# Kernel optimization log

Measured on AMD Instinct MI355X. Metric: run time of the kernel, lower is better.

The kernel has to match this reference:

```python
import jax, jax.numpy as jnp
import numpy as np

DIM, HEADS, B, S = 128, 4, 8, 80
BN_SCALE = np.float32(1.0 / np.sqrt(1.0 + 1e-5))  # eval-mode BatchNorm2d with running stats (0, 1)


def conv2d(x, w, b=None, groups=1, pad=0):
    y = jax.lax.conv_general_dilated(x, w, (1, 1), [(pad, pad), (pad, pad)],
                                     dimension_numbers=('NCHW', 'OIHW', 'NCHW'),
                                     feature_group_count=groups)
    return y if b is None else y + b[None, :, None, None]


def gate(x, w1, b1, g, bt, w2, b2):
    # Conv1x1 -> BatchNorm2d(eval) -> ReLU -> Conv1x1 -> Sigmoid
    y = conv2d(x, w1, b1)
    y = y * (g * BN_SCALE)[None, :, None, None] + bt[None, :, None, None]
    return jax.nn.sigmoid(conv2d(jax.nn.relu(y), w2, b2))


def layernorm(x, w, b):
    # Restormer WithBias LayerNorm over the channel dim
    mu = jnp.mean(x, 1, keepdims=True)
    var = jnp.var(x, 1, keepdims=True)
    return (x - mu) / jnp.sqrt(var + 1e-5) * w[None, :, None, None] + b[None, :, None, None]


def l2norm(x):
    # F.normalize(dim=-1) incl. complex: divide by L2 norm of |x|
    n = jnp.sqrt(jnp.sum(jnp.abs(x) ** 2, -1, keepdims=True))
    return x / jnp.maximum(n, 1e-12)


def split_heads(t):
    b, c, h, w = t.shape
    return t.reshape(b, HEADS, c // HEADS, h * w)


def _etb(x, ln1_w, ln1_b, ln2_w, ln2_b,
         f_temp, f_proj_w, f_w1, f_wb1, f_bn_g, f_bn_b, f_w2, f_wb2,
         s_temp, s_q1_w, s_q1_b, s_k1_w, s_k1_b, s_v1_w, s_v1_b,
         s_q3_w, s_q5_w, s_k3_w, s_k5_w, s_v3_w, s_v5_w, s_c3_w, s_c5_w, s_proj_w,
         ff_dw1_w, ff_dw2_w, ff_proj_w,
         ffg_w1, ffg_b1, ffg_bng, ffg_bnb, ffg_w2, ffg_b2,
         ffg1_w1, ffg1_b1, ffg1_bng, ffg1_bnb, ffg1_w2, ffg1_b2):
    b, c, h, w = x.shape
    G = c // 2
    xn = layernorm(x, ln1_w, ln1_b)
    # ---- Attention_F (the repeated fft2(x) calls in torch are identical; computed once) ----
    xf = jnp.fft.fft2(xn)
    qf = l2norm(split_heads(xf))  # q_f == k_f in the original code
    vf = split_heads(xf)
    attn = jnp.einsum('bhcn,bhdn->bhcd', qf, qf) * f_temp
    attn = jax.nn.softmax(attn.real, -1) + 1j * jax.nn.softmax(attn.imag, -1)
    # NOTE: torch applies ifft2 over the LAST TWO dims of [b, head, c, h*w] -> (c, h*w)
    out_f = jnp.abs(jnp.fft.ifft2(jnp.einsum('bhcd,bhdn->bhcn', attn, vf))).reshape(b, c, h, w)
    out_f_l = jnp.abs(jnp.fft.ifft2(gate(xf.real, f_w1, f_wb1, f_bn_g, f_bn_b, f_w2, f_wb2) * xf))
    a_f = conv2d(jnp.concatenate([out_f, out_f_l], 1), f_proj_w)
    # ---- Attention_S ----
    q1 = conv2d(xn, s_q1_w, s_q1_b)
    k1 = conv2d(xn, s_k1_w, s_k1_b)
    v1 = conv2d(xn, s_v1_w, s_v1_b)
    qs = jnp.concatenate([conv2d(q1, s_q3_w, groups=G, pad=1), conv2d(q1, s_q5_w, groups=G, pad=2)], 1)
    ks = jnp.concatenate([conv2d(k1, s_k3_w, groups=G, pad=1), conv2d(k1, s_k5_w, groups=G, pad=2)], 1)
    vs = jnp.concatenate([conv2d(v1, s_v3_w, groups=G, pad=1), conv2d(v1, s_v5_w, groups=G, pad=2)], 1)
    qn = l2norm(split_heads(qs))
    kn = l2norm(split_heads(ks))
    vh = split_heads(vs)
    attn_s = jax.nn.softmax(jnp.einsum('bhcn,bhdn->bhcd', qn, kn) * s_temp, -1)
    out_s = jnp.einsum('bhcd,bhdn->bhcn', attn_s, vh).reshape(b, c, h, w)
    out_s_l = jnp.concatenate([conv2d(xn, s_c3_w, groups=G, pad=1), conv2d(xn, s_c5_w, groups=G, pad=2)], 1)
    a_s = conv2d(jnp.concatenate([out_s, out_s_l], 1), s_proj_w)
    x = x + a_f + a_s
    # ---- FeedForward ----
    xn2 = layernorm(x, ln2_w, ln2_b)
    xf2 = jnp.fft.fft2(xn2)
    x_f = jnp.abs(gate(xf2.real, ffg_w1, ffg_b1, ffg_bng, ffg_bnb, ffg_w2, ffg_b2) * xf2)
    x_f_g = jax.nn.gelu(x_f, approximate=False) * x_f
    x_s = conv2d(xn2, ff_dw1_w, groups=c, pad=1)
    x_s_g = jax.nn.gelu(x_s, approximate=False) * x_s
    cat = jnp.concatenate([x_f_g, x_s_g], 1)  # [b, 2c, h, w]
    cf = jnp.fft.fft2(cat)
    x_f2b = jnp.abs(jnp.fft.ifft2(gate(cf.real, ffg1_w1, ffg1_b1, ffg1_bng, ffg1_bnb, ffg1_w2, ffg1_b2) * cf))
    x_s2b = conv2d(cat, ff_dw2_w, groups=c, pad=1)
    return x + conv2d(jnp.concatenate([x_f2b, x_s2b], 1), ff_proj_w)


def setup_inputs() -> dict:
    key = jax.random.key(0)
    ks = iter(jax.random.split(key, 64))
    rn = lambda shape, s=0.02: jax.random.normal(next(ks), shape, jnp.float32) * s
    d = {}
    d['x'] = jax.random.normal(next(ks), (B, DIM, S, S), jnp.float32)
    for n in ('ln1_w', 'ln2_w'):
        d[n] = jnp.ones((DIM,), jnp.float32)
    for n in ('ln1_b', 'ln2_b'):
        d[n] = jnp.zeros((DIM,), jnp.float32)
    d['f_temp'] = jnp.ones((HEADS, 1, 1), jnp.float32)
    d['s_temp'] = jnp.ones((HEADS, 1, 1), jnp.float32)
    d['f_proj_w'] = rn((DIM, 2 * DIM, 1, 1))
    d['s_proj_w'] = rn((DIM, 2 * DIM, 1, 1))
    r = DIM // 16
    d['f_w1'] = rn((r, DIM, 1, 1)); d['f_wb1'] = jnp.zeros((r,), jnp.float32)
    d['f_bn_g'] = jnp.ones((r,), jnp.float32); d['f_bn_b'] = jnp.zeros((r,), jnp.float32)
    d['f_w2'] = rn((DIM, r, 1, 1)); d['f_wb2'] = jnp.zeros((DIM,), jnp.float32)
    for n in ('s_q1', 's_k1', 's_v1'):
        d[n + '_w'] = rn((DIM, DIM, 1, 1)); d[n + '_b'] = jnp.zeros((DIM,), jnp.float32)
    for n in ('s_q3', 's_k3', 's_v3', 's_c3'):
        d[n + '_w'] = rn((DIM // 2, 2, 3, 3))
    for n in ('s_q5', 's_k5', 's_v5', 's_c5'):
        d[n + '_w'] = rn((DIM // 2, 2, 5, 5))
    d['ff_dw1_w'] = rn((DIM, 1, 3, 3))
    d['ff_dw2_w'] = rn((2 * DIM, 2, 3, 3))
    d['ff_proj_w'] = rn((DIM, 4 * DIM, 1, 1))
    d['ffg_w1'] = rn((r, DIM, 1, 1)); d['ffg_b1'] = jnp.zeros((r,), jnp.float32)
    d['ffg_bng'] = jnp.ones((r,), jnp.float32); d['ffg_bnb'] = jnp.zeros((r,), jnp.float32)
    d['ffg_w2'] = rn((DIM, r, 1, 1)); d['ffg_b2'] = jnp.zeros((DIM,), jnp.float32)
    d['ffg1_w1'] = rn((r, 2 * DIM, 1, 1)); d['ffg1_b1'] = jnp.zeros((r,), jnp.float32)
    d['ffg1_bng'] = jnp.ones((r,), jnp.float32); d['ffg1_bnb'] = jnp.zeros((r,), jnp.float32)
    d['ffg1_w2'] = rn((2 * DIM, r, 1, 1)); d['ffg1_b2'] = jnp.zeros((2 * DIM,), jnp.float32)
    return d


def reference(x, ln1_w, ln1_b, ln2_w, ln2_b,
              f_temp, f_proj_w, f_w1, f_wb1, f_bn_g, f_bn_b, f_w2, f_wb2,
              s_temp, s_q1_w, s_q1_b, s_k1_w, s_k1_b, s_v1_w, s_v1_b,
              s_q3_w, s_q5_w, s_k3_w, s_k5_w, s_v3_w, s_v5_w, s_c3_w, s_c5_w, s_proj_w,
              ff_dw1_w, ff_dw2_w, ff_proj_w,
              ffg_w1, ffg_b1, ffg_bng, ffg_bnb, ffg_w2, ffg_b2,
              ffg1_w1, ffg1_b1, ffg1_bng, ffg1_bnb, ffg1_w2, ffg1_b2):
    return _etb(x, ln1_w, ln1_b, ln2_w, ln2_b,
                f_temp, f_proj_w, f_w1, f_wb1, f_bn_g, f_bn_b, f_w2, f_wb2,
                s_temp, s_q1_w, s_q1_b, s_k1_w, s_k1_b, s_v1_w, s_v1_b,
                s_q3_w, s_q5_w, s_k3_w, s_k5_w, s_v3_w, s_v5_w, s_c3_w, s_c5_w, s_proj_w,
                ff_dw1_w, ff_dw2_w, ff_proj_w,
                ffg_w1, ffg_b1, ffg_bng, ffg_bnb, ffg_w2, ffg_b2,
                ffg1_w1, ffg1_b1, ffg1_bng, ffg1_bnb, ffg1_w2, ffg1_b2)
```

## Files before the change

### kernel.cpp

```cpp
#include <hip/hip_runtime.h>
#include <math.h>

#define DI __device__ __forceinline__

constexpr int B_ = 8, C_ = 128, H_ = 4, S_ = 80, N_ = 6400;
constexpr int P_ = B_ * N_;
constexpr int NSPL = 2;
constexpr float PI2 = 6.283185307179586f;
constexpr float BN_SC = 0.9999950000374997f;

typedef __attribute__((ext_vector_type(8))) short bf16x8;
typedef __attribute__((ext_vector_type(4))) float f32x4;

DI void cfma(float2& a, float2 u, float2 v) {
  a.x = fmaf(u.x, v.x, a.x); a.x = fmaf(-u.y, v.y, a.x);
  a.y = fmaf(u.x, v.y, a.y); a.y = fmaf(u.y, v.x, a.y);
}
DI float2 cmul(float2 u, float2 v) {
  return make_float2(u.x * v.x - u.y * v.y, u.x * v.y + u.y * v.x);
}
DI float gelu_mul(float m) {
  return 0.5f * m * (1.f + erff(m * 0.7071067811865476f)) * m;
}
DI unsigned short bf16_rn(float f) {
  union { float f; unsigned int u; } v; v.f = f;
  unsigned int u = v.u;
  return (unsigned short)((u + 0x7fffu + ((u >> 16) & 1u)) >> 16);
}

__global__ __launch_bounds__(256) void k_layernorm(const float* __restrict__ in,
    const float* __restrict__ w, const float* __restrict__ bb, float* __restrict__ out) {
  __shared__ float redS[4][64], redS2[4][64];
  __shared__ float muv[64], invv[64];
  const int tid = threadIdx.x;
  const int g = tid >> 6, l = tid & 63;
  const int p = blockIdx.x * 64 + l;
  const int b = p / N_, n = p % N_;
  const float* xp = in + (size_t)b * C_ * N_ + n;
  float s = 0.f, s2 = 0.f;
  for (int c = g * 32; c < g * 32 + 32; c++) {
    float v = xp[(size_t)c * N_];
    s += v; s2 = fmaf(v, v, s2);
  }
  redS[g][l] = s; redS2[g][l] = s2;
  __syncthreads();
  if (g == 0) {
    float ts  = redS[0][l] + redS[1][l] + redS[2][l] + redS[3][l];
    float ts2 = redS2[0][l] + redS2[1][l] + redS2[2][l] + redS2[3][l];
    float mu = ts * (1.f / C_);
    float var = ts2 * (1.f / C_) - mu * mu;
    muv[l] = mu; invv[l] = rsqrtf(var + 1e-5f);
  }
  __syncthreads();
  const float mu = muv[l], inv = invv[l];
  float* op = out + (size_t)b * C_ * N_ + n;
  for (int c = g * 32; c < g * 32 + 32; c++) {
    float v = xp[(size_t)c * N_];
    op[(size_t)c * N_] = (v - mu) * inv * w[c] + bb[c];
  }
}


__global__ __launch_bounds__(256) void k_fft2_r2c(const float* __restrict__ in, float2* __restrict__ out,
                                                  int nCh, int inCtot, int inCoff,
                                                  float2* __restrict__ out2, int inCoff2, int nimg,
                                                  float* __restrict__ nrm) {
  __shared__ float2 data[N_];
  __shared__ float2 tw[80];
  int img = blockIdx.x;
  float2* op;
  int coff;
  if (img >= nimg) { img -= nimg; op = out2 + (size_t)img * N_; coff = inCoff2; }
  else { op = out + (size_t)img * N_; coff = inCoff; }
  const int b = img / nCh, ch = img % nCh;
  const float* ip = in + ((size_t)b * inCtot + coff + ch) * N_;
  const int tid = threadIdx.x;
  float* dataR = (float*)data;
  if (tid < 80) { float a = -PI2 * (float)tid * (1.f / 80.f); float sv, cv; sincosf(a, &sv, &cv); tw[tid] = make_float2(cv, sv); }
  for (int i = tid; i < N_; i += 256) dataR[i] = ip[i];
  __syncthreads();
  const int r0 = (tid >> 4) * 5;
  const int cg = tid & 15;
  float2 a1[5][3];
  for (int j = 0; j < 5; j++)
    for (int i = 0; i < 3; i++) a1[j][i] = make_float2(0.f, 0.f);
  {
    int idx[3] = {0, 0, 0};
    for (int c = 0; c < 80; ++c) {
      float d[5]; float2 t[3];
      #pragma unroll
      for (int j = 0; j < 5; j++) d[j] = dataR[(r0 + j) * 80 + c];
      #pragma unroll
      for (int i = 0; i < 3; i++) t[i] = tw[idx[i]];
      #pragma unroll
      for (int j = 0; j < 5; j++) {
        #pragma unroll
        for (int i = 0; i < 3; i++) {
          a1[j][i].x = fmaf(d[j], t[i].x, a1[j][i].x);
          a1[j][i].y = fmaf(d[j], t[i].y, a1[j][i].y);
        }
      }
      #pragma unroll
      for (int i = 0; i < 3; i++) { idx[i] += cg + 16 * i; if (idx[i] >= 80) idx[i] -= 80; }
    }
  }
  __syncthreads();
  #pragma unroll
  for (int i = 0; i < 3; i++) {
    const int k = cg + 16 * i;
    #pragma unroll
    for (int j = 0; j < 5; j++) {
      if (k <= 40) data[(r0 + j) * 80 + k] = a1[j][i];
      if (k >= 1 && k <= 39) data[(r0 + j) * 80 + 80 - k] = make_float2(a1[j][i].x, -a1[j][i].y);
    }
  }
  __syncthreads();
  const int k0 = (tid & 15) * 5;
  const int rg = tid >> 4;
  float2 a2[3][5];
  for (int j = 0; j < 3; j++)
    for (int i = 0; i < 5; i++) a2[j][i] = make_float2(0.f, 0.f);
  {
    int idx[3] = {0, 0, 0};
    for (int r = 0; r < 80; ++r) {
      float2 d[5]; float2 t[3];
      #pragma unroll
      for (int i = 0; i < 5; i++) d[i] = data[r * 80 + k0 + i];
      #pragma unroll
      for (int j = 0; j < 3; j++) t[j] = tw[idx[j]];
      #pragma unroll
      for (int j = 0; j < 3; j++) {
        #pragma unroll
        for (int i = 0; i < 5; i++) cfma(a2[j][i], d[i], t[j]);
      }
      #pragma unroll
      for (int j = 0; j < 3; j++) { idx[j] += rg + 16 * j; if (idx[j] >= 80) idx[j] -= 80; }
    }
  }
  #pragma unroll
  for (int j = 0; j < 3; j++) {
    const int k1 = rg + 16 * j;
    #pragma unroll
    for (int i = 0; i < 5; i++) {
      const int k2 = k0 + i;
      if (k1 <= 40) op[k1 * 80 + k2] = a2[j][i];
      if (k1 >= 1 && k1 <= 39) {
        const int m2 = (k2 == 0) ? 0 : 80 - k2;
        op[(80 - k1) * 80 + m2] = make_float2(a2[j][i].x, -a2[j][i].y);
      }
    }
  }
  if (nrm) {
    float s = 0.f;
    #pragma unroll
    for (int j = 0; j < 3; j++) {
      const int k1 = rg + 16 * j;
      if (k1 <= 40) {
        const float wgt = (k1 == 0 || k1 == 40) ? 1.f : 2.f;
        #pragma unroll
        for (int i = 0; i < 5; i++)
          s += wgt * (a2[j][i].x * a2[j][i].x + a2[j][i].y * a2[j][i].y);
      }
    }
    __syncthreads();
    float* red = (float*)data;
    red[tid] = s;
    __syncthreads();
    for (int st = 128; st > 0; st >>= 1) { if (tid < st) red[tid] += red[tid + st]; __syncthreads(); }
    if (tid == 0) nrm[img] = fmaxf(sqrtf(red[0]), 1e-12f);
  }
}

__global__ __launch_bounds__(256) void k_ifft2_abs(const float2* __restrict__ in, float* __restrict__ out,
                                                   int inC, int outCtot, int outCoff,
                                                   const float2* __restrict__ in2, int outCoff2, int nimg) {
  __shared__ float2 data[N_];
  __shared__ float2 tw[80];
  int img = blockIdx.x;
  const float2* ip;
  int coff;
  if (img >= nimg) { img -= nimg; ip = in2 + (size_t)img * N_; coff = outCoff2; }
  else { ip = in + (size_t)img * N_; coff = outCoff; }
  const int b = img / inC, ch = img % inC;
  float* op = out + ((size_t)b * outCtot + coff + ch) * N_;
  const int tid = threadIdx.x;
  if (tid < 80) { float a = PI2 * (float)tid * (1.f / 80.f); float sv, cv; sincosf(a, &sv, &cv); tw[tid] = make_float2(cv, sv); }
  for (int i = tid; i < N_; i += 256) data[i] = ip[i];
  __syncthreads();
  const int rg = tid >> 4;
  const int cg = tid & 15;
  float2 E[3][3], O[3][3];
  for (int j = 0; j < 3; j++)
    for (int i = 0; i < 3; i++) { E[j][i] = make_float2(0.f, 0.f); O[j][i] = make_float2(0.f, 0.f); }
  {
    int idx[3], inc[3];
    #pragma unroll
    for (int i = 0; i < 3; i++) { idx[i] = 0; inc[i] = (2 * (cg + 16 * i)) % 80; }
    for (int m = 0; m < 40; ++m) {
      float4 z[3]; float2 t[3];
      #pragma unroll
      for (int j = 0; j < 3; j++) z[j] = *(const float4*)&data[(rg + 16 * j) * 80 + 2 * m];
      #pragma unroll
      for (int i = 0; i < 3; i++) t[i] = tw[idx[i]];
      #pragma unroll
      for (int j = 0; j < 3; j++) {
        float2 ze = make_float2(z[j].x, z[j].y);
        float2 zo = make_float2(z[j].z, z[j].w);
        #pragma unroll
        for (int i = 0; i < 3; i++) { cfma(E[j][i], ze, t[i]); cfma(O[j][i], zo, t[i]); }
      }
      #pragma unroll
      for (int i = 0; i < 3; i++) { idx[i] += inc[i]; if (idx[i] >= 80) idx[i] -= 80; }
    }
  }
  __syncthreads();
  #pragma unroll
  for (int j = 0; j < 3; j++) {
    const int r = rg + 16 * j;
    if (r <= 40) {
      #pragma unroll
      for (int i = 0; i < 3; i++) {
        const int n2 = cg + 16 * i;
        if (n2 < 40) {
          float2 u = cmul(tw[n2], O[j][i]);
          data[r * 80 + n2]      = make_float2(E[j][i].x + u.x, E[j][i].y + u.y);
          data[r * 80 + n2 + 40] = make_float2(E[j][i].x - u.x, E[j][i].y - u.y);
        }
      }
    }
  }
  __syncthreads();
  const int r0 = (tid >> 4) * 5;
  const int k0 = (tid & 15) * 5;
  float accR[5][5];
  for (int j = 0; j < 5; j++)
    for (int i = 0; i < 5; i++) accR[j][i] = 0.f;
  {
    int idx[5];
    #pragma unroll
    for (int j = 0; j < 5; j++) idx[j] = r0 + j;
    for (int r = 1; r <= 39; ++r) {
      float2 d[5]; float2 t[5];
      #pragma unroll
      for (int i = 0; i < 5; i++) d[i] = data[r * 80 + k0 + i];
      #pragma unroll
      for (int j = 0; j < 5; j++) t[j] = tw[idx[j]];
      #pragma unroll
      for (int j = 0; j < 5; j++) {
        #pragma unroll
        for (int i = 0; i < 5; i++) {
          accR[j][i] = fmaf(t[j].x, d[i].x, accR[j][i]);
          accR[j][i] = fmaf(-t[j].y, d[i].y, accR[j][i]);
        }
      }
      #pragma unroll
      for (int j = 0; j < 5; j++) { idx[j] += r0 + j; if (idx[j] >= 80) idx[j] -= 80; }
    }
  }
  #pragma unroll
  for (int i = 0; i < 5; i++) {
    float2 b0 = data[k0 + i];
    float2 b40 = data[40 * 80 + k0 + i];
    #pragma unroll
    for (int j = 0; j < 5; j++) {
      float s40 = ((r0 + j) & 1) ? -b40.x : b40.x;
      float res = 2.f * accR[j][i] + b0.x + s40;
      op[(r0 + j) * 80 + k0 + i] = fabsf(res) * (1.f / (float)N_);
    }
  }
}

__global__ __launch_bounds__(256) void k_iff_combo(const float2* __restrict__ in6400, float* __restrict__ out6400,
                                                   const float2* __restrict__ inF, float* __restrict__ outF) {
  __shared__ float2 data[N_];
  __shared__ float2 tw[80];
  __shared__ float2 tws[80];
  const int tid = threadIdx.x;
  if (blockIdx.x < (unsigned)(B_ * C_)) {
    const int row = blockIdx.x;
    const float2* ip = in6400 + (size_t)row * N_;
    float* op = out6400 + (size_t)row * N_;
    if (tid < 80) {
      float a = PI2 * (float)tid * (1.f / 80.f); float sv, cv; sincosf(a, &sv, &cv); tw[tid] = make_float2(cv, sv);
      float a2 = PI2 * (float)tid * (1.f / 6400.f); sincosf(a2, &sv, &cv); tws[tid] = make_float2(cv, sv);
    }
    for (int i = tid; i < N_; i += 256) data[i] = ip[i];
    __syncthreads();
    {
      const int r0 = (tid >> 4) * 5;
      const int cg = tid & 15;
      float2 E[5][3], O[5][3];
      for (int j = 0; j < 5; j++)
        for (int i = 0; i < 3; i++) { E[j][i] = make_float2(0.f, 0.f); O[j][i] = make_float2(0.f, 0.f); }
      int idx[3], inc[3];
      #pragma unroll
      for (int i = 0; i < 3; i++) { idx[i] = 0; inc[i] = (2 * (cg + 16 * i)) % 80; }
      for (int m = 0; m < 40; ++m) {
        float2 xe[5], xo[5], t[3];
        #pragma unroll
        for (int j = 0; j < 5; j++) {
          xe[j] = data[(r0 + j) + 160 * m];
          xo[j] = data[(r0 + j) + 160 * m + 80];
        }
        #pragma unroll
        for (int i = 0; i < 3; i++) t[i] = tw[idx[i]];
        #pragma unroll
        for (int j = 0; j < 5; j++) {
          #pragma unroll
          for (int i = 0; i < 3; i++) { cfma(E[j][i], xe[j], t[i]); cfma(O[j][i], xo[j], t[i]); }
        }
        #pragma unroll
        for (int i = 0; i < 3; i++) { idx[i] += inc[i]; if (idx[i] >= 80) idx[i] -= 80; }
      }
      __syncthreads();
      #pragma unroll
      for (int j = 0; j < 5; j++) {
        const int k1 = r0 + j;
        #pragma unroll
        for (int i = 0; i < 3; i++) {
          const int n2 = cg + 16 * i;
          if (n2 < 40) {
            float2 u = cmul(tw[n2], O[j][i]);
            float2 Ap = make_float2(E[j][i].x + u.x, E[j][i].y + u.y);
            float2 Am = make_float2(E[j][i].x - u.x, E[j][i].y - u.y);
            int t6 = k1 * n2; int q = t6 / 80, s6 = t6 - q * 80;
            data[k1 * 80 + n2] = cmul(Ap, cmul(tw[q], tws[s6]));
            int t6b = k1 * (n2 + 40); int qb = t6b / 80, sb = t6b - qb * 80;
            data[k1 * 80 + n2 + 40] = cmul(Am, cmul(tw[qb], tws[sb]));
          }
        }
      }
    }
    __syncthreads();
    {
      const int rg5 = tid >> 3;
      const int cg5 = tid & 7;
      float2 E2[5][3], O2[5][3];
      for (int i = 0; i < 5; i++)
        for (int j = 0; j < 3; j++) { E2[i][j] = make_float2(0.f, 0.f); O2[i][j] = make_float2(0.f, 0.f); }
      int idx[5], inc[5];
      #pragma unroll
      for (int i = 0; i < 5; i++) { idx[i] = 0; inc[i] = (2 * (cg5 * 5 + i)) % 80; }
      int n2c[3];
      #pragma unroll
      for (int j = 0; j < 3; j++) { int n2 = rg5 + 32 * j; n2c[j] = (n2 < 80) ? n2 : 0; }
      for (int m = 0; m < 40; ++m) {
        float2 ae[3], ao[3], t[5];
        #pragma unroll
        for (int j = 0; j < 3; j++) {
          ae[j] = data[(2 * m) * 80 + n2c[j]];
          ao[j] = data[(2 * m + 1) * 80 + n2c[j]];
        }
        #pragma unroll
        for (int i = 0; i < 5; i++) t[i] = tw[idx[i]];
        #pragma unroll
        for (int i = 0; i < 5; i++) {
          #pragma unroll
          for (int j = 0; j < 3; j++) { cfma(E2[i][j], ae[j], t[i]); cfma(O2[i][j], ao[j], t[i]); }
        }
        #pragma unroll
        for (int i = 0; i < 5; i++) { idx[i] += inc[i]; if (idx[i] >= 80) idx[i] -= 80; }
      }
      #pragma unroll
      for (int i = 0; i < 5; i++) {
        const int n1 = cg5 * 5 + i;
        #pragma unroll
        for (int j = 0; j < 3; j++) {
          const int n2 = rg5 + 32 * j;
          if (n2 < 80) {
            float2 u = cmul(tw[n1], O2[i][j]);
            float2 o1 = make_float2(E2[i][j].x + u.x, E2[i][j].y + u.y);
            float2 o2 = make_float2(E2[i][j].x - u.x, E2[i][j].y - u.y);
            op[n1 * 80 + n2] = sqrtf(o1.x * o1.x + o1.y * o1.y) * (1.f / 6400.f);
            op[(n1 + 40) * 80 + n2] = sqrtf(o2.x * o2.x + o2.y * o2.y) * (1.f / 6400.f);
          }
        }
      }
    }
  } else {
    const int img = blockIdx.x - B_ * C_;
    const float2* ip = inF + (size_t)img * N_;
    float* op = outF + (size_t)img * N_;
    if (tid < 80) { float a = PI2 * (float)tid * (1.f / 80.f); float sv, cv; sincosf(a, &sv, &cv); tw[tid] = make_float2(cv, sv); }
    for (int i = tid; i < N_; i += 256) data[i] = ip[i];
    __syncthreads();
    const int rg = tid >> 4;
    const int cg = tid & 15;
    float2 E[3][3], O[3][3];
    for (int j = 0; j < 3; j++)
      for (int i = 0; i < 3; i++) { E[j][i] = make_float2(0.f, 0.f); O[j][i] = make_float2(0.f, 0.f); }
    {
      int idx[3], inc[3];
      #pragma unroll
      for (int i = 0; i < 3; i++) { idx[i] = 0; inc[i] = (2 * (cg + 16 * i)) % 80; }
      for (int m = 0; m < 40; ++m) {
        float4 z[3]; float2 t[3];
        #pragma unroll
        for (int j = 0; j < 3; j++) z[j] = *(const float4*)&data[(rg + 16 * j) * 80 + 2 * m];
        #pragma unroll
        for (int i = 0; i < 3; i++) t[i] = tw[idx[i]];
        #pragma unroll
        for (int j = 0; j < 3; j++) {
          float2 ze = make_float2(z[j].x, z[j].y);
          float2 zo = make_float2(z[j].z, z[j].w);
          #pragma unroll
          for (int i = 0; i < 3; i++) { cfma(E[j][i], ze, t[i]); cfma(O[j][i], zo, t[i]); }
        }
        #pragma unroll
        for (int i = 0; i < 3; i++) { idx[i] += inc[i]; if (idx[i] >= 80) idx[i] -= 80; }
      }
    }
    __syncthreads();
    #pragma unroll
    for (int j = 0; j < 3; j++) {
      const int r = rg + 16 * j;
      if (r <= 40) {
        #pragma unroll
        for (int i = 0; i < 3; i++) {
          const int n2 = cg + 16 * i;
          if (n2 < 40) {
            float2 u = cmul(tw[n2], O[j][i]);
            data[r * 80 + n2]      = make_float2(E[j][i].x + u.x, E[j][i].y + u.y);
            data[r * 80 + n2 + 40] = make_float2(E[j][i].x - u.x, E[j][i].y - u.y);
          }
        }
      }
    }
    __syncthreads();
    const int r0 = (tid >> 4) * 5;
    const int k0 = (tid & 15) * 5;
    float accR[5][5];
    for (int j = 0; j < 5; j++)
      for (int i = 0; i < 5; i++) accR[j][i] = 0.f;
    {
      int idx[5];
      #pragma unroll
      for (int j = 0; j < 5; j++) idx[j] = r0 + j;
      for (int r = 1; r <= 39; ++r) {
        float2 d[5]; float2 t[5];
        #pragma unroll
        for (int i = 0; i < 5; i++) d[i] = data[r * 80 + k0 + i];
        #pragma unroll
        for (int j = 0; j < 5; j++) t[j] = tw[idx[j]];
        #pragma unroll
        for (int j = 0; j < 5; j++) {
          #pragma unroll
          for (int i = 0; i < 5; i++) {
            accR[j][i] = fmaf(t[j].x, d[i].x, accR[j][i]);
            accR[j][i] = fmaf(-t[j].y, d[i].y, accR[j][i]);
          }
        }
        #pragma unroll
        for (int j = 0; j < 5; j++) { idx[j] += r0 + j; if (idx[j] >= 80) idx[j] -= 80; }
      }
    }
    #pragma unroll
    for (int i = 0; i < 5; i++) {
      float2 b0 = data[k0 + i];
      float2 b40 = data[40 * 80 + k0 + i];
      #pragma unroll
      for (int j = 0; j < 5; j++) {
        float s40 = ((r0 + j) & 1) ? -b40.x : b40.x;
        float res = 2.f * accR[j][i] + b0.x + s40;
        op[(r0 + j) * 80 + k0 + i] = fabsf(res) * (1.f / (float)N_);
      }
    }
  }
}

// ... 646 lines not shown
```

Measured before the change: 1.127 ms.

## Factor 80-point DFT in r2c FFT kernel into 16x5 Cooley-Tukey stages

Replaces the direct O(N^2) 80-point DFTs along rows and columns in the forward real-to-complex FFT2 kernel with a two-stage decomposition: 16-point DFTs over stride-5 subsequences, then a 5-point combine with twiddles. This cuts the multiply-add count per output and the twiddle lookups from shared memory. It raises register use (5x5 complex accumulators) and changes the thread-to-frequency mapping, which could affect occupancy and numerical rounding slightly.

New measurement: 1.041 ms. -7.7%, faster.

```diff
diff --git a/kernel.cpp b/kernel.cpp
--- a/kernel.cpp
+++ b/kernel.cpp
@@ -79,92 +79,104 @@
   if (tid < 80) { float a = -PI2 * (float)tid * (1.f / 80.f); float sv, cv; sincosf(a, &sv, &cv); tw[tid] = make_float2(cv, sv); }
   for (int i = tid; i < N_; i += 256) dataR[i] = ip[i];
   __syncthreads();
-  const int r0 = (tid >> 4) * 5;
-  const int cg = tid & 15;
-  float2 a1[5][3];
-  for (int j = 0; j < 5; j++)
-    for (int i = 0; i < 3; i++) a1[j][i] = make_float2(0.f, 0.f);
+  const int rg = tid >> 4;
+  const int kap = tid & 15;
+  const int r0 = rg * 5;
   {
-    int idx[3] = {0, 0, 0};
-    for (int c = 0; c < 80; ++c) {
-      float d[5]; float2 t[3];
-      #pragma unroll
-      for (int j = 0; j < 5; j++) d[j] = dataR[(r0 + j) * 80 + c];
-      #pragma unroll
-      for (int i = 0; i < 3; i++) t[i] = tw[idx[i]];
+    float2 F[5][5];
+    #pragma unroll
+    for (int j = 0; j < 5; j++)
+      #pragma unroll
+      for (int q = 0; q < 5; q++) F[j][q] = make_float2(0.f, 0.f);
+    int m16 = 0;
+    for (int m = 0; m < 16; ++m) {
+      float2 t = tw[5 * m16];
       #pragma unroll
       for (int j = 0; j < 5; j++) {
-        #pragma unroll
-        for (int i = 0; i < 3; i++) {
-          a1[j][i].x = fmaf(d[j], t[i].x, a1[j][i].x);
-          a1[j][i].y = fmaf(d[j], t[i].y, a1[j][i].y);
-        }
-      }
-      #pragma unroll
-      for (int i = 0; i < 3; i++) { idx[i] += cg + 16 * i; if (idx[i] >= 80) idx[i] -= 80; }
-    }
-  }
-  __syncthreads();
-  #pragma unroll
-  for (int i = 0; i < 3; i++) {
-    const int k = cg + 16 * i;
-    #pragma unroll
-    for (int j = 0; j < 5; j++) {
-      if (k <= 40) data[(r0 + j) * 80 + k] = a1[j][i];
-      if (k >= 1 && k <= 39) data[(r0 + j) * 80 + 80 - k] = make_float2(a1[j][i].x, -a1[j][i].y);
+        const float* row = &dataR[(r0 + j) * 80 + 5 * m];
+        #pragma unroll
+        for (int q = 0; q < 5; q++) {
+          float xv = row[q];
+          F[j][q].x = fmaf(xv, t.x, F[j][q].x);
+          F[j][q].y = fmaf(xv, t.y, F[j][q].y);
+        }
+      }
+      m16 += kap; if (m16 >= 16) m16 -= 16;
+    }
+    __syncthreads();
+    #pragma unroll
+    for (int s = 0; s < 5; ++s) {
+      const int k = kap + 16 * s;
+      if (k <= 40) {
+        float2 t1 = tw[k];
+        float2 t2 = tw[(2 * k) % 80];
+        float2 t3 = tw[(3 * k) % 80];
+        float2 t4 = tw[(4 * k) % 80];
+        #pragma unroll
+        for (int j = 0; j < 5; j++) {
+          float2 a = F[j][0];
+          cfma(a, F[j][1], t1);
+          cfma(a, F[j][2], t2);
+          cfma(a, F[j][3], t3);
+          cfma(a, F[j][4], t4);
+          data[(r0 + j) * 80 + k] = a;
+          if (k >= 1 && k <= 39) data[(r0 + j) * 80 + 80 - k] = make_float2(a.x, -a.y);
+        }
+      }
     }
   }
   __syncthreads();
   const int k0 = (tid & 15) * 5;
-  const int rg = tid >> 4;
-  float2 a2[3][5];
-  for (int j = 0; j < 3; j++)
-    for (int i = 0; i < 5; i++) a2[j][i] = make_float2(0.f, 0.f);
+  const int kap2 = tid >> 4;
+  float snrm = 0.f;
   {
-    int idx[3] = {0, 0, 0};
-    for (int r = 0; r < 80; ++r) {
-      float2 d[5]; float2 t[3];
-      #pragma unroll
-      for (int i = 0; i < 5; i++) d[i] = data[r * 80 + k0 + i];
-      #pragma unroll
-      for (int j = 0; j < 3; j++) t[j] = tw[idx[j]];
-      #pragma unroll
-      for (int j = 0; j < 3; j++) {
-        #pragma unroll
-        for (int i = 0; i < 5; i++) cfma(a2[j][i], d[i], t[j]);
-      }
-      #pragma unroll
-      for (int j = 0; j < 3; j++) { idx[j] += rg + 16 * j; if (idx[j] >= 80) idx[j] -= 80; }
-    }
-  }
-  #pragma unroll
-  for (int j = 0; j < 3; j++) {
-    const int k1 = rg + 16 * j;
-    #pragma unroll
-    for (int i = 0; i < 5; i++) {
-      const int k2 = k0 + i;
-      if (k1 <= 40) op[k1 * 80 + k2] = a2[j][i];
-      if (k1 >= 1 && k1 <= 39) {
-        const int m2 = (k2 == 0) ? 0 : 80 - k2;
-        op[(80 - k1) * 80 + m2] = make_float2(a2[j][i].x, -a2[j][i].y);
+    float2 G[5][5];
+    #pragma unroll
+    for (int q = 0; q < 5; q++)
+      #pragma unroll
+      for (int i = 0; i < 5; i++) G[q][i] = make_float2(0.f, 0.f);
+    int m16 = 0;
+    for (int m = 0; m < 16; ++m) {
+      float2 t = tw[5 * m16];
+      #pragma unroll
+      for (int q = 0; q < 5; q++) {
+        const float2* rowp = &data[(5 * m + q) * 80 + k0];
+        #pragma unroll
+        for (int i = 0; i < 5; i++) cfma(G[q][i], rowp[i], t);
+      }
+      m16 += kap2; if (m16 >= 16) m16 -= 16;
+    }
+    #pragma unroll
+    for (int s = 0; s < 5; ++s) {
+      const int k1 = kap2 + 16 * s;
+      if (k1 <= 40) {
+        float2 t1 = tw[k1];
+        float2 t2 = tw[(2 * k1) % 80];
+        float2 t3 = tw[(3 * k1) % 80];
+        float2 t4 = tw[(4 * k1) % 80];
+        const float wgt = (k1 == 0 || k1 == 40) ? 1.f : 2.f;
+        #pragma unroll
+        for (int i = 0; i < 5; i++) {
+          float2 y = G[0][i];
+          cfma(y, G[1][i], t1);
+          cfma(y, G[2][i], t2);
+          cfma(y, G[3][i], t3);
+          cfma(y, G[4][i], t4);
+          const int k2 = k0 + i;
+          op[k1 * 80 + k2] = y;
+          if (k1 >= 1 && k1 <= 39) {
+            const int m2 = (k2 == 0) ? 0 : 80 - k2;
+            op[(80 - k1) * 80 + m2] = make_float2(y.x, -y.y);
+          }
+          snrm += wgt * (y.x * y.x + y.y * y.y);
+        }
       }
     }
   }
   if (nrm) {
-    float s = 0.f;
-    #pragma unroll
-    for (int j = 0; j < 3; j++) {
-      const int k1 = rg + 16 * j;
-      if (k1 <= 40) {
-        const float wgt = (k1 == 0 || k1 == 40) ? 1.f : 2.f;
-        #pragma unroll
-        for (int i = 0; i < 5; i++)
-          s += wgt * (a2[j][i].x * a2[j][i].x + a2[j][i].y * a2[j][i].y);
-      }
-    }
     __syncthreads();
     float* red = (float*)data;
-    red[tid] = s;
+    red[tid] = snrm;
     __syncthreads();
     for (int st = 128; st > 0; st >>= 1) { if (tid < st) red[tid] += red[tid + st]; __syncthreads(); }
     if (tid == 0) nrm[img] = fmaxf(sqrtf(red[0]), 1e-12f);
```
